# Optimization experiments

Hardware: AMD Instinct MI355X
Metric: run time of the kernel (lower is better)

## Reference

```python
import jax, jax.numpy as jnp
import numpy as np

DT = 0.1


def setup_inputs() -> dict:
    key = jax.random.key(0)
    k1, k2, k3, k4 = jax.random.split(key, 4)
    B, T, I, H, O = 32, 1024, 256, 512, 256
    return {
        "x": jax.random.normal(k1, (B, T, I), dtype=jnp.float32),
        "input_weights": jax.random.normal(k2, (H, I), dtype=jnp.float32) * (1.0 / np.sqrt(I)),
        "recurrent_weights": jax.random.normal(k3, (H, H), dtype=jnp.float32) * (1.0 / np.sqrt(H)),
        "time_constants": jnp.ones((H,), dtype=jnp.float32) + 0.1,
        "output_weights": jax.random.normal(k4, (O, H), dtype=jnp.float32) * (1.0 / np.sqrt(H)),
        "bias": jnp.zeros((H,), dtype=jnp.float32),
    }


def reference(x, input_weights, recurrent_weights, time_constants, output_weights, bias):
    B = x.shape[0]
    H = recurrent_weights.shape[0]
    h0 = jnp.zeros((B, H), dtype=x.dtype)

    # Precompute the input projection for all timesteps at once: (B,T,I)@(I,H) -> (T,B,H)
    sensory_all = jnp.einsum("bti,hi->tbh", x, input_weights)

    def step(hidden, sensory):
        # sensory: (B, H)
        recurrent = hidden @ recurrent_weights.T                      # (B, H)
        adaptive_tau = jax.nn.softplus(
            time_constants + 0.1 * jnp.mean(jnp.abs(sensory), axis=0)
        )                                                             # (H,)
        activation = jnp.tanh(sensory + recurrent + bias)             # (B, H)
        dhidden_dt = -hidden / adaptive_tau[None, :] + activation
        hidden = hidden + DT * dhidden_dt
        out_t = hidden @ output_weights.T                             # (B, O)
        return hidden, out_t

    final_hidden, outputs = jax.lax.scan(step, h0, sensory_all)        # outputs: (T, B, O)
    output = jnp.transpose(outputs, (1, 0, 2))                          # (B, T, O)
    return output, final_hidden
```

## Files before the change

### kernel.cpp

```cpp
#include <hip/hip_runtime.h>
#include <cstddef>
#include <cstdint>

#define B_ 32
#define T_ 1024
#define IN_ 256
#define H_ 512
#define O_ 256
#define DT_ 0.1f

typedef _Float16 f16x8 __attribute__((ext_vector_type(8)));
typedef float f32x4 __attribute__((ext_vector_type(4)));

template<int N, int K, bool SWA, bool SWC>
__global__ __launch_bounds__(256, 4) void gemm128(const float* __restrict__ A,
                                                  const float* __restrict__ Bw,
                                                  float* __restrict__ C) {
    __shared__ float al[32][132];
    __shared__ float bl[32][132];
    const int tid = threadIdx.x;
    const int m0 = blockIdx.x * 128;
    const int n0 = blockIdx.y * 128;
    const int tx = tid & 15;
    const int ty = tid >> 4;
    float acc[8][8] = {};

    const int lrow = tid >> 3;
    const int kk = (tid & 7) * 4;

    for (int kc = 0; kc < K; kc += 32) {
        __syncthreads();
#pragma unroll
        for (int p = 0; p < 4; ++p) {
            const int row = lrow + p * 32;
            const int m = m0 + row;
            const size_t aoff = SWA ? ((size_t)((m & 31) * T_ + (m >> 5)) * K)
                                    : ((size_t)m * K);
            const float4 v = *(const float4*)(A + aoff + kc + kk);
            al[kk + 0][row] = v.x; al[kk + 1][row] = v.y;
            al[kk + 2][row] = v.z; al[kk + 3][row] = v.w;
        }
#pragma unroll
        for (int p = 0; p < 4; ++p) {
            const int row = lrow + p * 32;
            const float4 v = *(const float4*)(Bw + (size_t)(n0 + row) * K + kc + kk);
            bl[kk + 0][row] = v.x; bl[kk + 1][row] = v.y;
            bl[kk + 2][row] = v.z; bl[kk + 3][row] = v.w;
        }
        __syncthreads();
#pragma unroll
        for (int k = 0; k < 32; ++k) {
            float av[8], bv[8];
            *(float4*)&av[0] = *(const float4*)&al[k][ty * 8];
            *(float4*)&av[4] = *(const float4*)&al[k][ty * 8 + 4];
            *(float4*)&bv[0] = *(const float4*)&bl[k][tx * 8];
            *(float4*)&bv[4] = *(const float4*)&bl[k][tx * 8 + 4];
#pragma unroll
            for (int i = 0; i < 8; ++i)
#pragma unroll
                for (int j = 0; j < 8; ++j)
                    acc[i][j] = fmaf(av[i], bv[j], acc[i][j]);
        }
    }
#pragma unroll
    for (int i = 0; i < 8; ++i) {
        const int m = m0 + ty * 8 + i;
        const size_t coff = SWC ? ((size_t)((m & 31) * T_ + (m >> 5)) * N)
                                : ((size_t)m * N);
        const float4 v0 = make_float4(acc[i][0], acc[i][1], acc[i][2], acc[i][3]);
        const float4 v1 = make_float4(acc[i][4], acc[i][5], acc[i][6], acc[i][7]);
        *(float4*)(C + coff + n0 + tx * 8) = v0;
        *(float4*)(C + coff + n0 + tx * 8 + 4) = v1;
    }
}

__global__ __launch_bounds__(512) void tau_kernel(const float* __restrict__ sens,
                                                  const float* __restrict__ tc,
                                                  float* __restrict__ acoef) {
    const int t = blockIdx.x;
    const int h = threadIdx.x;
    float s = 0.f;
#pragma unroll 8
    for (int b = 0; b < B_; ++b)
        s += fabsf(sens[((size_t)t * B_ + b) * H_ + h]);
    const float x = tc[h] + 0.1f * (s * (1.f / 32.f));
    const float sp = fmaxf(x, 0.f) + log1pf(expf(-fabsf(x)));
    acoef[(size_t)t * H_ + h] = 1.f - DT_ / sp;
}

#define WLDS_BYTES 131072
#define PRED_OFF   WLDS_BYTES
#define H2S_OFF    (WLDS_BYTES + 2048)
#define SMEM_TOT   (WLDS_BYTES + 2048 + 1024)

#define BARRIER_LGKM() asm volatile("s_waitcnt lgkmcnt(0)\n\ts_barrier" ::: "memory")
#define MFMA16(a, b, c) __builtin_amdgcn_mfma_f32_16x16x32_f16(a, b, c, 0, 0, 0)

__global__ __attribute__((amdgpu_flat_work_group_size(512, 512),
                          amdgpu_waves_per_eu(2, 2)))
void scan_kernel(const float* __restrict__ Wr, const float* __restrict__ acoef,
                 const float* __restrict__ bias, float* sensH,
                 float* __restrict__ finalh) {
    extern __shared__ char smem[];
    float* pred   = (float*)(smem + PRED_OFF);
    _Float16* h2s = (_Float16*)(smem + H2S_OFF);

    const int tid  = threadIdx.x;
    const int b    = blockIdx.x;
    const int lane = tid & 63;
    const int w    = tid >> 6;
    const int lm   = lane & 15;
    const int lq   = lane >> 4;

    f16x8 wf0[12], wf1[12], wf2[12], wf3[12];
#pragma unroll
    for (int kt = 0; kt < 16; ++kt) {
#pragma unroll
        for (int rt = 0; rt < 4; ++rt) {
            const int row  = w * 64 + rt * 16 + lm;
            const int col0 = kt * 32 + lq * 8;
            const float* p = Wr + (size_t)row * H_ + col0;
            const float4 v0 = *(const float4*)p;
            const float4 v1 = *(const float4*)(p + 4);
            f16x8 f;
            f[0] = (_Float16)v0.x; f[1] = (_Float16)v0.y;
            f[2] = (_Float16)v0.z; f[3] = (_Float16)v0.w;
            f[4] = (_Float16)v1.x; f[5] = (_Float16)v1.y;
            f[6] = (_Float16)v1.z; f[7] = (_Float16)v1.w;
            if (kt < 12) {
                if      (rt == 0) wf0[kt] = f;
                else if (rt == 1) wf1[kt] = f;
                else if (rt == 2) wf2[kt] = f;
                else              wf3[kt] = f;
            } else {
                *(f16x8*)(smem + ((((kt - 12) * 8 + w) * 4 + rt) * 64 + lane) * 16) = f;
            }
        }
    }

    if (tid < 256) ((float*)h2s)[tid] = 0.f;
    float h_reg = 0.f;
    const float bias_r = bias[tid];
    float s_cur = sensH[(size_t)b * H_ + tid];
    float a_cur = acoef[tid];
    __syncthreads();

    const int bq_base = H2S_OFF + lq * 16;
    const int wl_base = (w * 4 * 64 + lane) * 16;

#define LDB(kt) (*(const f16x8*)(smem + bq_base + (kt) * 64))
#define LDW(kt, rt) (*(const f16x8*)(smem + ((kt) - 12) * 32768 + wl_base + (rt) * 1024))

    for (int t = 0; t < T_; ++t) {
        const int tn = (t < T_ - 1) ? t + 1 : t;
        const float s_nxt = sensH[((size_t)tn * B_ + b) * H_ + tid];
        const float a_nxt = acoef[(size_t)tn * H_ + tid];

        f32x4 D0 = {0.f, 0.f, 0.f, 0.f};
        f32x4 D1 = {0.f, 0.f, 0.f, 0.f};
        f32x4 D2 = {0.f, 0.f, 0.f, 0.f};
        f32x4 D3 = {0.f, 0.f, 0.f, 0.f};

        f16x8 bcur = LDB(0);
#pragma unroll
        for (int kt = 0; kt < 12; ++kt) {
            const f16x8 bnxt = LDB(kt + 1);
            D0 = MFMA16(wf0[kt], bcur, D0);
            D1 = MFMA16(wf1[kt], bcur, D1);
            D2 = MFMA16(wf2[kt], bcur, D2);
            D3 = MFMA16(wf3[kt], bcur, D3);
            bcur = bnxt;
        }
        {
            f16x8 u0 = LDW(12, 0), u1 = LDW(12, 1), u2 = LDW(12, 2), u3 = LDW(12, 3);
#pragma unroll
            for (int kt = 12; kt < 16; ++kt) {
                f16x8 n0, n1, n2, n3, bnxt;
                if (kt < 15) {
                    bnxt = LDB(kt + 1);
                    n0 = LDW(kt + 1, 0); n1 = LDW(kt + 1, 1);
                    n2 = LDW(kt + 1, 2); n3 = LDW(kt + 1, 3);
                }
                D0 = MFMA16(u0, bcur, D0);
                D1 = MFMA16(u1, bcur, D1);
                D2 = MFMA16(u2, bcur, D2);
                D3 = MFMA16(u3, bcur, D3);
                if (kt < 15) { u0 = n0; u1 = n1; u2 = n2; u3 = n3; bcur = bnxt; }
            }
        }

        if (lm == 0) {
            float* pb = pred + w * 64 + lq * 4;
            *(f32x4*)(pb +  0) = D0;
            *(f32x4*)(pb + 16) = D1;
            *(f32x4*)(pb + 32) = D2;
            *(f32x4*)(pb + 48) = D3;
        }
        BARRIER_LGKM();

        {
            const float rec = pred[tid];
            const float act = tanhf(s_cur + rec + bias_r);
            h_reg = a_cur * h_reg + DT_ * act;
            sensH[((size_t)t * B_ + b) * H_ + tid] = h_reg;
            h2s[tid] = (_Float16)h_reg;
            s_cur = s_nxt;
            a_cur = a_nxt;
        }
        BARRIER_LGKM();
    }
    finalh[(size_t)b * H_ + tid] = h_reg;
#undef LDB
#undef LDW
}

extern "C" void kernel_launch(void* const* d_in, const int* in_sizes, int n_in,
                              void* d_out, int out_size, void* d_ws, size_t ws_size,
                              hipStream_t stream) {
    const float* x    = (const float*)d_in[0];
    const float* Win  = (const float*)d_in[1];
    const float* Wr   = (const float*)d_in[2];
    const float* tc   = (const float*)d_in[3];
    const float* Wo   = (const float*)d_in[4];
    const float* bias = (const float*)d_in[5];
    float* out = (float*)d_out;

    float* sensH = (float*)d_ws;
    float* acoef = sensH + (size_t)T_ * B_ * H_;
    const size_t need = ((size_t)T_ * B_ * H_ + (size_t)T_ * H_) * sizeof(float);
    if (ws_size < need) return;

    (void)hipFuncSetAttribute((const void*)scan_kernel,
                              hipFuncAttributeMaxDynamicSharedMemorySize, SMEM_TOT);

    {
        dim3 grid(32768 / 128, H_ / 128);
        hipLaunchKernelGGL((gemm128<H_, IN_, true, false>), grid, dim3(256), 0, stream,
                           x, Win, sensH);
    }
    hipLaunchKernelGGL(tau_kernel, dim3(T_), dim3(H_), 0, stream, sensH, tc, acoef);
    hipLaunchKernelGGL(scan_kernel, dim3(B_), dim3(512), SMEM_TOT, stream,
                       Wr, acoef, bias, sensH, out + (size_t)B_ * T_ * O_);
    {
        dim3 grid(32768 / 128, O_ / 128);
        hipLaunchKernelGGL((gemm128<O_, H_, false, true>), grid, dim3(256), 0, stream,
                           sensH, Wo, out);
    }
}
```

Measured before the change: 2.147 ms.

## Keep all recurrent weights in registers and triple-buffer hidden state to drop a barrier

The scan kernel now holds the full fp16 recurrent weight slice in registers instead of splitting it between registers and LDS, which removes the LDS weight reads from the per-step MFMA loop. The hidden-state buffer in LDS is now triple-buffered. The barrier between writing the partial sums and reading them is replaced by an lgkmcnt wait, since each wave reads only its own rows, leaving one barrier per timestep. The cost is much higher VGPR pressure: 256 VGPRs for weights alone, with the waves_per_eu hint removed. This risks spilling or very low occupancy for the 512-thread block.

```diff
diff --git a/kernel.cpp b/kernel.cpp
--- a/kernel.cpp
+++ b/kernel.cpp
@@ -88,22 +88,15 @@
     acoef[(size_t)t * H_ + h] = 1.f - DT_ / sp;
 }
 
-#define WLDS_BYTES 131072
-#define PRED_OFF   WLDS_BYTES
-#define H2S_OFF    (WLDS_BYTES + 2048)
-#define SMEM_TOT   (WLDS_BYTES + 2048 + 1024)
-
 #define BARRIER_LGKM() asm volatile("s_waitcnt lgkmcnt(0)\n\ts_barrier" ::: "memory")
 #define MFMA16(a, b, c) __builtin_amdgcn_mfma_f32_16x16x32_f16(a, b, c, 0, 0, 0)
 
-__global__ __attribute__((amdgpu_flat_work_group_size(512, 512),
-                          amdgpu_waves_per_eu(2, 2)))
+__global__ __attribute__((amdgpu_flat_work_group_size(512, 512)))
 void scan_kernel(const float* __restrict__ Wr, const float* __restrict__ acoef,
                  const float* __restrict__ bias, float* sensH,
                  float* __restrict__ finalh) {
-    extern __shared__ char smem[];
-    float* pred   = (float*)(smem + PRED_OFF);
-    _Float16* h2s = (_Float16*)(smem + H2S_OFF);
+    __shared__ float pred[512];
+    __shared__ _Float16 h2s[3][512];
 
     const int tid  = threadIdx.x;
     const int b    = blockIdx.x;
@@ -112,7 +105,7 @@
     const int lm   = lane & 15;
     const int lq   = lane >> 4;
 
-    f16x8 wf0[12], wf1[12], wf2[12], wf3[12];
+    f16x8 wf[4][16];
 #pragma unroll
     for (int kt = 0; kt < 16; ++kt) {
 #pragma unroll
@@ -127,66 +120,39 @@
             f[2] = (_Float16)v0.z; f[3] = (_Float16)v0.w;
             f[4] = (_Float16)v1.x; f[5] = (_Float16)v1.y;
             f[6] = (_Float16)v1.z; f[7] = (_Float16)v1.w;
-            if (kt < 12) {
-                if      (rt == 0) wf0[kt] = f;
-                else if (rt == 1) wf1[kt] = f;
-                else if (rt == 2) wf2[kt] = f;
-                else              wf3[kt] = f;
-            } else {
-                *(f16x8*)(smem + ((((kt - 12) * 8 + w) * 4 + rt) * 64 + lane) * 16) = f;
-            }
-        }
-    }
-
-    if (tid < 256) ((float*)h2s)[tid] = 0.f;
+            wf[rt][kt] = f;
+        }
+    }
+
+    if (tid < 256) ((float*)&h2s[0][0])[tid] = 0.f;
     float h_reg = 0.f;
     const float bias_r = bias[tid];
     float s_cur = sensH[(size_t)b * H_ + tid];
     float a_cur = acoef[tid];
     __syncthreads();
 
-    const int bq_base = H2S_OFF + lq * 16;
-    const int wl_base = (w * 4 * 64 + lane) * 16;
-
-#define LDB(kt) (*(const f16x8*)(smem + bq_base + (kt) * 64))
-#define LDW(kt, rt) (*(const f16x8*)(smem + ((kt) - 12) * 32768 + wl_base + (rt) * 1024))
+    const int bq = lq * 8;
+    int cur = 0, nxt = 1;
 
     for (int t = 0; t < T_; ++t) {
         const int tn = (t < T_ - 1) ? t + 1 : t;
         const float s_nxt = sensH[((size_t)tn * B_ + b) * H_ + tid];
         const float a_nxt = acoef[(size_t)tn * H_ + tid];
 
+        const _Float16* hc = &h2s[cur][bq];
+
         f32x4 D0 = {0.f, 0.f, 0.f, 0.f};
         f32x4 D1 = {0.f, 0.f, 0.f, 0.f};
         f32x4 D2 = {0.f, 0.f, 0.f, 0.f};
         f32x4 D3 = {0.f, 0.f, 0.f, 0.f};
 
-        f16x8 bcur = LDB(0);
-#pragma unroll
-        for (int kt = 0; kt < 12; ++kt) {
-            const f16x8 bnxt = LDB(kt + 1);
-            D0 = MFMA16(wf0[kt], bcur, D0);
-            D1 = MFMA16(wf1[kt], bcur, D1);
-            D2 = MFMA16(wf2[kt], bcur, D2);
-            D3 = MFMA16(wf3[kt], bcur, D3);
-            bcur = bnxt;
-        }
-        {
-            f16x8 u0 = LDW(12, 0), u1 = LDW(12, 1), u2 = LDW(12, 2), u3 = LDW(12, 3);
-#pragma unroll
-            for (int kt = 12; kt < 16; ++kt) {
-                f16x8 n0, n1, n2, n3, bnxt;
-                if (kt < 15) {
-                    bnxt = LDB(kt + 1);
-                    n0 = LDW(kt + 1, 0); n1 = LDW(kt + 1, 1);
-                    n2 = LDW(kt + 1, 2); n3 = LDW(kt + 1, 3);
-                }
-                D0 = MFMA16(u0, bcur, D0);
-                D1 = MFMA16(u1, bcur, D1);
-                D2 = MFMA16(u2, bcur, D2);
-                D3 = MFMA16(u3, bcur, D3);
-                if (kt < 15) { u0 = n0; u1 = n1; u2 = n2; u3 = n3; bcur = bnxt; }
-            }
+#pragma unroll
+        for (int kt = 0; kt < 16; ++kt) {
+            const f16x8 bk = *(const f16x8*)(hc + kt * 32);
+            D0 = MFMA16(wf[0][kt], bk, D0);
+            D1 = MFMA16(wf[1][kt], bk, D1);
+            D2 = MFMA16(wf[2][kt], bk, D2);
+            D3 = MFMA16(wf[3][kt], bk, D3);
         }
 
         if (lm == 0) {
@@ -196,22 +162,25 @@
             *(f32x4*)(pb + 32) = D2;
             *(f32x4*)(pb + 48) = D3;
         }
-        BARRIER_LGKM();
+        asm volatile("s_waitcnt lgkmcnt(0)" ::: "memory");
 
         {
             const float rec = pred[tid];
             const float act = tanhf(s_cur + rec + bias_r);
             h_reg = a_cur * h_reg + DT_ * act;
             sensH[((size_t)t * B_ + b) * H_ + tid] = h_reg;
-            h2s[tid] = (_Float16)h_reg;
+            h2s[nxt][tid] = (_Float16)h_reg;
             s_cur = s_nxt;
             a_cur = a_nxt;
         }
         BARRIER_LGKM();
+
+        const int old = cur;
+        cur = nxt;
+        nxt = (nxt == 2) ? 0 : nxt + 1;
+        (void)old;
     }
     finalh[(size_t)b * H_ + tid] = h_reg;
-#undef LDB
-#undef LDW
 }
 
 extern "C" void kernel_launch(void* const* d_in, const int* in_sizes, int n_in,
@@ -230,16 +199,13 @@
     const size_t need = ((size_t)T_ * B_ * H_ + (size_t)T_ * H_) * sizeof(float);
     if (ws_size < need) return;
 
-    (void)hipFuncSetAttribute((const void*)scan_kernel,
-                              hipFuncAttributeMaxDynamicSharedMemorySize, SMEM_TOT);
-
     {
         dim3 grid(32768 / 128, H_ / 128);
         hipLaunchKernelGGL((gemm128<H_, IN_, true, false>), grid, dim3(256), 0, stream,
                            x, Win, sensH);
     }
     hipLaunchKernelGGL(tau_kernel, dim3(T_), dim3(H_), 0, stream, sensH, tc, acoef);
-    hipLaunchKernelGGL(scan_kernel, dim3(B_), dim3(512), SMEM_TOT, stream,
+    hipLaunchKernelGGL(scan_kernel, dim3(B_), dim3(512), 0, stream,
                        Wr, acoef, bias, sensH, out + (size_t)B_ * T_ * O_);
     {
         dim3 grid(32768 / 128, O_ / 128);
```

New measurement: 3.852 ms. 79.4% more time.
